# Performance work log

Hardware: AMD Instinct MI355X
Metric: run time of the kernel (lower is better)

Reference implementation:

```python
import jax, jax.numpy as jnp
import numpy as np

EPS = 1e-5

def _bn(x, gamma, beta):
    # BatchNorm with track_running_stats=False: batch stats over all dims but last
    axes = tuple(range(x.ndim - 1))
    mu = jnp.mean(x, axis=axes)
    var = jnp.var(x, axis=axes)  # biased, as torch uses for normalization
    return (x - mu) * jax.lax.rsqrt(var + EPS) * gamma + beta

def setup_inputs() -> dict:
    B, N, D = 8, 200, 128
    key = jax.random.key(0)
    ks = jax.random.split(key, 14)
    s = 1.0 / np.sqrt(D)
    def w(k):
        return jax.random.uniform(k, (D, D), jnp.float32, -s, s)
    def b(k):
        return jax.random.uniform(k, (D,), jnp.float32, -s, s)
    return {
        'h': jax.random.normal(ks[0], (B, N, D), jnp.float32),
        'e': jax.random.normal(ks[1], (B, N, N, D), jnp.float32),
        'Uw': w(ks[2]), 'Ub': b(ks[3]),
        'Vw': w(ks[4]), 'Vb': b(ks[5]),
        'Aw': w(ks[6]), 'Ab': b(ks[7]),
        'Bw': w(ks[8]), 'Bb': b(ks[9]),
        'Cw': w(ks[10]), 'Cb': b(ks[11]),
        'gamma_h': jnp.ones((D,), jnp.float32), 'beta_h': jnp.zeros((D,), jnp.float32),
        'gamma_e': jnp.ones((D,), jnp.float32), 'beta_e': jnp.zeros((D,), jnp.float32),
    }

def reference(h, e, Uw, Ub, Vw, Vb, Aw, Ab, Bw, Bb, Cw, Cb,
              gamma_h, beta_h, gamma_e, beta_e):
    h_in, e_in = h, e
    Uh = h @ Uw.T + Ub                      # [B,N,D]
    Vh = h @ Vw.T + Vb                      # [B,N,D]
    Ah = h @ Aw.T + Ab
    Bh = h @ Bw.T + Bb
    Ce = e @ Cw.T + Cb                      # [B,N,N,D]
    # e_new[b,i,j,d] = Ah[b,j,d] + Bh[b,i,d] + Ce[b,i,j,d]
    e_new = Ah[:, None, :, :] + Bh[:, :, None, :] + Ce
    gates = jax.nn.sigmoid(e_new)           # [B,N,N,D]
    # sum aggregation over source nodes j with Vh broadcast over i
    agg = jnp.sum(gates * Vh[:, None, :, :], axis=2)  # [B,N,D]
    h_new = Uh + agg
    h_out = h_in + jax.nn.relu(_bn(h_new, gamma_h, beta_h))
    e_out = e_in + jax.nn.relu(_bn(e_new, gamma_e, beta_e))
    return (h_out, e_out)
```

## Files before the change

kernel.cpp:

```cpp
#include <hip/hip_runtime.h>
#include <hip/hip_bf16.h>


#define B_ 8
#define N_ 200
#define D_ 128
#define BN_ (B_*N_)
#define HN_ (BN_*D_)

typedef __attribute__((ext_vector_type(8))) short short8v;
typedef __attribute__((ext_vector_type(4))) short short4v;
typedef __attribute__((ext_vector_type(4))) float float4v;
typedef __attribute__((ext_vector_type(4))) unsigned int uint4v;

__device__ __forceinline__ unsigned short f2b(float f) {
  unsigned u = __float_as_uint(f);
  u += 0x7FFFu + ((u >> 16) & 1u);
  return (unsigned short)(u >> 16);
}

__global__ __launch_bounds__(256) void prelin_kernel(
    const float* __restrict__ h,
    const float* __restrict__ Uw, const float* __restrict__ Ub,
    const float* __restrict__ Vw, const float* __restrict__ Vb,
    const float* __restrict__ Aw, const float* __restrict__ Ab,
    const float* __restrict__ Bw, const float* __restrict__ Bb,
    const float* __restrict__ Cw,
    float* __restrict__ Uh, float* __restrict__ Vh,
    float* __restrict__ Ah, float* __restrict__ Bh,
    unsigned short* __restrict__ Cwf) {
  const int tid = threadIdx.x;
  if (blockIdx.x >= 100) {
    const int slot = (blockIdx.x - 100) * 256 + tid;
    const int fr = slot >> 6, ln = slot & 63;
    const int t = fr >> 2, l = fr & 3, cc = ln & 15, qq = ln >> 4;
    const float* src = Cw + (t * 16 + cc) * 128 + l * 32 + qq * 8;
    float4v v0 = *(const float4v*)src;
    float4v v1 = *(const float4v*)(src + 4);
    short8v s;
    s[0] = (short)f2b(v0.x); s[1] = (short)f2b(v0.y);
    s[2] = (short)f2b(v0.z); s[3] = (short)f2b(v0.w);
    s[4] = (short)f2b(v1.x); s[5] = (short)f2b(v1.y);
    s[6] = (short)f2b(v1.z); s[7] = (short)f2b(v1.w);
    *(short8v*)(Cwf + (size_t)slot * 8) = s;
    return;
  }
  const int r0 = blockIdx.x * 16;
  __shared__ float hs[16][128];
  for (int k = 0; k < 2; k++) {
    int g = k * 256 + tid;
    int row = g >> 5, col4 = g & 31;
    *(float4v*)&hs[row][col4 * 4] =
        *(const float4v*)(h + (size_t)(r0 + row) * D_ + col4 * 4);
  }
  __syncthreads();
  const int c0 = tid, c1 = tid + 256;
  const float* w0 = (c0 < 128) ? (Uw + c0 * 128) : (Vw + (c0 - 128) * 128);
  const float  b0 = (c0 < 128) ? Ub[c0] : Vb[c0 - 128];
  const float* w1 = (c1 < 384) ? (Aw + (c1 - 256) * 128) : (Bw + (c1 - 384) * 128);
  const float  b1 = (c1 < 384) ? Ab[c1 - 256] : Bb[c1 - 384];
  float acc0[16], acc1[16];
#pragma unroll
  for (int r = 0; r < 16; r++) { acc0[r] = 0.f; acc1[r] = 0.f; }
  for (int k = 0; k < 128; k += 4) {
    float4v w0v = *(const float4v*)(w0 + k);
    float4v w1v = *(const float4v*)(w1 + k);
#pragma unroll
    for (int r = 0; r < 16; r++) {
      float4v hv = *(const float4v*)&hs[r][k];
      acc0[r] = fmaf(hv.x, w0v.x, fmaf(hv.y, w0v.y, fmaf(hv.z, w0v.z, fmaf(hv.w, w0v.w, acc0[r]))));
      acc1[r] = fmaf(hv.x, w1v.x, fmaf(hv.y, w1v.y, fmaf(hv.z, w1v.z, fmaf(hv.w, w1v.w, acc1[r]))));
    }
  }
  float* dst0 = (c0 < 128) ? Uh : Vh; const int cc0 = c0 & 127;
  float* dst1 = (c1 < 384) ? Ah : Bh; const int cc1 = (c1 - 256) & 127;
#pragma unroll
  for (int r = 0; r < 16; r++) {
    dst0[(size_t)(r0 + r) * D_ + cc0] = acc0[r] + b0;
    dst1[(size_t)(r0 + r) * D_ + cc1] = acc1[r] + b1;
  }
}

template <int MODE>
__global__ __launch_bounds__(256, 4) void gemm_pass(
    const float* __restrict__ e, const unsigned short* __restrict__ Cwf,
    const float* __restrict__ Cb, const float* __restrict__ Ah,
    const float* __restrict__ Bh, const float* __restrict__ Vh,
    float* __restrict__ agg, float* __restrict__ psum, float* __restrict__ psumsq,
    const float* __restrict__ scale_e, const float* __restrict__ shift_e,
    float* __restrict__ e_out) {
  const int tid = threadIdx.x;
  const int blk = blockIdx.x;
  const int bi = blk >> 2, jt = blk & 3;
  const int b = bi / N_;
  const int lane = tid & 63, wz = tid >> 6;
  const int c = lane & 15, q = lane >> 4;
  const int j0 = jt * 64;

  __shared__ __align__(16) unsigned short Bs[16384];
  __shared__ float base_s[128];
  __shared__ float ss_s[256];

  const int jrow = j0 + wz * 16 + c;
  const bool rok = (jrow < N_);
  const float* ep = e + ((size_t)bi * N_ + jrow) * D_ + q * 8;
  float4v ef[8];
#pragma unroll
  for (int l = 0; l < 4; l++) {
    ef[2 * l]     = rok ? *(const float4v*)(ep + l * 32)     : (float4v){0.f,0.f,0.f,0.f};
    ef[2 * l + 1] = rok ? *(const float4v*)(ep + l * 32 + 4) : (float4v){0.f,0.f,0.f,0.f};
  }

  {
    const uint4v* bsrc = (const uint4v*)Cwf;
    uint4v* bdst = (uint4v*)Bs;
#pragma unroll
    for (int k2 = 0; k2 < 8; k2++) bdst[k2 * 256 + tid] = bsrc[k2 * 256 + tid];
  }
  if (tid < 128) {
    base_s[tid] = Cb[tid] + Bh[(size_t)bi * D_ + tid];
    if (MODE == 1) { ss_s[tid] = scale_e[tid]; ss_s[128 + tid] = shift_e[tid]; }
  }

  short8v av[4];
#pragma unroll
  for (int l = 0; l < 4; l++) {
    float4v v0 = ef[2 * l], v1 = ef[2 * l + 1];
    short8v s;
    s[0] = (short)f2b(v0.x); s[1] = (short)f2b(v0.y);
    s[2] = (short)f2b(v0.z); s[3] = (short)f2b(v0.w);
    s[4] = (short)f2b(v1.x); s[5] = (short)f2b(v1.y);
    s[6] = (short)f2b(v1.z); s[7] = (short)f2b(v1.w);
    av[l] = s;
  }
  __syncthreads();

  float4v acc[8];
#pragma unroll
  for (int t = 0; t < 8; t++) acc[t] = (float4v){0.f, 0.f, 0.f, 0.f};
#pragma unroll
  for (int l = 0; l < 4; l++) {
#pragma unroll
    for (int t = 0; t < 8; t++) {
      short8v cw = *(const short8v*)&Bs[(((t * 4 + l) * 64) + lane) * 8];
      if (MODE == 0)
        acc[t] = __builtin_amdgcn_mfma_f32_16x16x32_bf16(av[l], cw, acc[t], 0, 0, 0);
      else
        acc[t] = __builtin_amdgcn_mfma_f32_16x16x32_bf16(cw, av[l], acc[t], 0, 0, 0);
    }
  }

  if (MODE == 0) {
    const float* AhB = Ah + (size_t)b * N_ * D_;
    const float* VhB = Vh + (size_t)b * N_ * D_;
#pragma unroll
    for (int t = 0; t < 8; t++) {
      const int n = t * 16 + c;
      const float bse = base_s[n];
      float at = 0.f, st = 0.f, qt = 0.f;
#pragma unroll
      for (int r = 0; r < 4; r++) {
        const int j = j0 + wz * 16 + q * 4 + r;
        if (j < N_) {
          float x = acc[t][r] + bse + AhB[(size_t)j * D_ + n];
          float g = __builtin_amdgcn_rcpf(1.0f + __expf(-x));
          at += g * VhB[(size_t)j * D_ + n];
          st += x; qt += x * x;
        }
      }
      at += __shfl_xor(at, 16); at += __shfl_xor(at, 32);
      st += __shfl_xor(st, 16); st += __shfl_xor(st, 32);
      qt += __shfl_xor(qt, 16); qt += __shfl_xor(qt, 32);
      if (lane < 16) {
        atomicAdd(&agg[(size_t)bi * D_ + n], at);
        atomicAdd(&psum[(size_t)bi * D_ + n], st);
        atomicAdd(&psumsq[(size_t)bi * D_ + n], qt);
      }
    }
  } else {
    const int j = j0 + wz * 16 + c;
    if (j < N_) {
      const float* AhB = Ah + (size_t)b * N_ * D_;
      const size_t rowoff = ((size_t)bi * N_ + j) * D_;
#pragma unroll
      for (int t = 0; t < 8; t++) {
        const int n4 = t * 16 + q * 4;
        float4v ah = *(const float4v*)(AhB + (size_t)j * D_ + n4);
        float4v bs4 = *(const float4v*)&base_s[n4];
        float4v sc4 = *(const float4v*)&ss_s[n4];
        float4v sh4 = *(const float4v*)&ss_s[128 + n4];
        float4v ein = *(const float4v*)(e + rowoff + n4);
        float4v o;
#pragma unroll
        for (int r = 0; r < 4; r++) {
          float x = acc[t][r] + bs4[r] + ah[r];
          float y = fmaxf(x * sc4[r] + sh4[r], 0.f);
          o[r] = ein[r] + y;
        }
        *(float4v*)(e_out + rowoff + n4) = o;
      }
    }
  }
}

__global__ __launch_bounds__(256) void stats_part(
    const float* __restrict__ psum, const float* __restrict__ psumsq,
    const float* __restrict__ Uh, const float* __restrict__ agg,
    float* __restrict__ partial) {
  const int t = threadIdx.x, blk = blockIdx.x;
  const int cg = t & 31, rs = t >> 5;
  float4v ps = {0,0,0,0}, pq = {0,0,0,0}, hs = {0,0,0,0}, hq = {0,0,0,0};
#pragma unroll
  for (int p = 0; p < 2; p++) {
    const int row = blk * 16 + p * 8 + rs;
    const size_t off = (size_t)row * D_ + cg * 4;
    float4v a = *(const float4v*)(psum + off);
    float4v bq = *(const float4v*)(psumsq + off);
    float4v u = *(const float4v*)(Uh + off);
    float4v g = *(const float4v*)(agg + off);
    ps += a; pq += bq;
    float4v hv = u + g;
    hs += hv; hq += hv * hv;
  }
  __shared__ float4v red[4][8][32];
  red[0][rs][cg] = ps; red[1][rs][cg] = pq; red[2][rs][cg] = hs; red[3][rs][cg] = hq;
  __syncthreads();
  if (t < 128) {
    const int s = t >> 5, g = t & 31;
    float4v acc = red[s][0][g];
#pragma unroll
    for (int r = 1; r < 8; r++) acc += red[s][r][g];
    *(float4v*)(partial + (size_t)blk * 512 + s * 128 + g * 4) = acc;
  }
}

__global__ __launch_bounds__(128) void stats_final(
    const float* __restrict__ partial,
    const float* __restrict__ gamma_h, const float* __restrict__ beta_h,
    const float* __restrict__ gamma_e, const float* __restrict__ beta_e,
    float* __restrict__ scale_e, float* __restrict__ shift_e,
    float* __restrict__ scale_h, float* __restrict__ shift_h) {
  const int n = threadIdx.x;
  float s = 0.f, sq = 0.f, hs = 0.f, hq = 0.f;
  for (int p = 0; p < 100; p++) {
    const float* base = partial + (size_t)p * 512;
    s += base[n]; sq += base[128 + n]; hs += base[256 + n]; hq += base[384 + n];
  }
  const float Me = 8.f * 200.f * 200.f;
  float mean = s / Me;
  float var = sq / Me - mean * mean;
  float sce = gamma_e[n] * rsqrtf(var + 1e-5f);
  scale_e[n] = sce; shift_e[n] = beta_e[n] - mean * sce;
  const float Mh = (float)BN_;
  float mh = hs / Mh;
  float vh = hq / Mh - mh * mh;
  float sch = gamma_h[n] * rsqrtf(vh + 1e-5f);
  scale_h[n] = sch; shift_h[n] = beta_h[n] - mh * sch;
}

__global__ __launch_bounds__(256) void hpath_kernel(
    const float* __restrict__ h, const float* __restrict__ Uh,
    const float* __restrict__ agg, const float* __restrict__ scale_h,
    const float* __restrict__ shift_h, float* __restrict__ h_out) {
  const int idx = blockIdx.x * 256 + threadIdx.x;
  float4v u = ((const float4v*)Uh)[idx];
  float4v a = ((const float4v*)agg)[idx];
  float4v hv = ((const float4v*)h)[idx];
  float4v sc = ((const float4v*)scale_h)[idx & 31];
  float4v sh = ((const float4v*)shift_h)[idx & 31];
  float4v o;
#pragma unroll
  for (int l = 0; l < 4; l++) {
    float y = fmaxf((u[l] + a[l]) * sc[l] + sh[l], 0.f);
    o[l] = hv[l] + y;
  }
  ((float4v*)h_out)[idx] = o;
}

extern "C" void kernel_launch(void* const* d_in, const int* in_sizes, int n_in,
                              void* d_out, int out_size, void* d_ws, size_t ws_size,
                              hipStream_t stream) {
  const float* h  = (const float*)d_in[0];
  const float* e  = (const float*)d_in[1];
  const float* Uw = (const float*)d_in[2];  const float* Ub = (const float*)d_in[3];
  const float* Vw = (const float*)d_in[4];  const float* Vb = (const float*)d_in[5];
  const float* Aw = (const float*)d_in[6];  const float* Ab = (const float*)d_in[7];
  const float* Bw = (const float*)d_in[8];  const float* Bb = (const float*)d_in[9];
  const float* Cw = (const float*)d_in[10]; const float* Cb = (const float*)d_in[11];
  const float* gamma_h = (const float*)d_in[12]; const float* beta_h = (const float*)d_in[13];
  const float* gamma_e = (const float*)d_in[14]; const float* beta_e = (const float*)d_in[15];

  float* ws = (float*)d_ws;
  float* Uh = ws + 0;
  float* Vh = ws + (size_t)HN_;
  float* Ah = ws + (size_t)HN_ * 2;
  float* Bh = ws + (size_t)HN_ * 3;
  float* agg = ws + (size_t)HN_ * 4;
  float* psum = ws + (size_t)HN_ * 5;
  float* psumsq = ws + (size_t)HN_ * 6;
  float* scale_e = ws + (size_t)HN_ * 7;
  float* shift_e = scale_e + 128;
  float* scale_h = scale_e + 256;
  float* shift_h = scale_e + 384;
  unsigned short* Cwf = (unsigned short*)(scale_e + 512);
  float* partial = scale_e + 512 + 8192;

  float* h_out = (float*)d_out;
  float* e_out = (float*)d_out + HN_;

  prelin_kernel<<<108, 256, 0, stream>>>(h, Uw, Ub, Vw, Vb, Aw, Ab, Bw, Bb, Cw,
                                         Uh, Vh, Ah, Bh, Cwf);
  hipMemsetAsync(agg, 0, (size_t)3 * HN_ * sizeof(float), stream);
  gemm_pass<0><<<BN_ * 4, 256, 0, stream>>>(e, Cwf, Cb, Ah, Bh, Vh,
                                            agg, psum, psumsq,
                                            nullptr, nullptr, nullptr);
  stats_part<<<100, 256, 0, stream>>>(psum, psumsq, Uh, agg, partial);
  stats_final<<<1, 128, 0, stream>>>(partial, gamma_h, beta_h, gamma_e, beta_e,
                                     scale_e, shift_e, scale_h, shift_h);
  hpath_kernel<<<200, 256, 0, stream>>>(h, Uh, agg, scale_h, shift_h, h_out);
  gemm_pass<1><<<BN_ * 4, 256, 0, stream>>>(e, Cwf, Cb, Ah, Bh, nullptr,
                                            nullptr, nullptr, nullptr,
                                            scale_e, shift_e, e_out);
}
```

Baseline: 495.1 us.

## Process a whole (b,i) row per block with register-prefetched e tiles

Each block now handles all 200 j rows of one (b,i) pair instead of a quarter of them. Each wave loops over four 16-row groups and prefetches the next group's e values into registers while the current one runs through MFMA. Per-row reductions are combined in shared memory and written directly, which removes the memset and the global atomics. The Cw tile is loaded into LDS once per row rather than four times, but the grid has four times fewer blocks and each thread holds more registers, which may reduce occupancy and latency hiding.

```diff
diff --git a/kernel.cpp b/kernel.cpp
--- a/kernel.cpp
+++ b/kernel.cpp
@@ -90,26 +90,16 @@
     const float* __restrict__ scale_e, const float* __restrict__ shift_e,
     float* __restrict__ e_out) {
   const int tid = threadIdx.x;
-  const int blk = blockIdx.x;
-  const int bi = blk >> 2, jt = blk & 3;
+  const int bi = blockIdx.x;
   const int b = bi / N_;
-  const int lane = tid & 63, wz = tid >> 6;
+  const int lane = tid & 63, wv = tid >> 6;
   const int c = lane & 15, q = lane >> 4;
-  const int j0 = jt * 64;
+  const int j0 = wv * 64;
 
   __shared__ __align__(16) unsigned short Bs[16384];
   __shared__ float base_s[128];
   __shared__ float ss_s[256];
-
-  const int jrow = j0 + wz * 16 + c;
-  const bool rok = (jrow < N_);
-  const float* ep = e + ((size_t)bi * N_ + jrow) * D_ + q * 8;
-  float4v ef[8];
-#pragma unroll
-  for (int l = 0; l < 4; l++) {
-    ef[2 * l]     = rok ? *(const float4v*)(ep + l * 32)     : (float4v){0.f,0.f,0.f,0.f};
-    ef[2 * l + 1] = rok ? *(const float4v*)(ep + l * 32 + 4) : (float4v){0.f,0.f,0.f,0.f};
-  }
+  __shared__ float red[3][4][128];
 
   {
     const uint4v* bsrc = (const uint4v*)Cwf;
@@ -122,83 +112,145 @@
     if (MODE == 1) { ss_s[tid] = scale_e[tid]; ss_s[128 + tid] = shift_e[tid]; }
   }
 
-  short8v av[4];
-#pragma unroll
-  for (int l = 0; l < 4; l++) {
-    float4v v0 = ef[2 * l], v1 = ef[2 * l + 1];
-    short8v s;
-    s[0] = (short)f2b(v0.x); s[1] = (short)f2b(v0.y);
-    s[2] = (short)f2b(v0.z); s[3] = (short)f2b(v0.w);
-    s[4] = (short)f2b(v1.x); s[5] = (short)f2b(v1.y);
-    s[6] = (short)f2b(v1.z); s[7] = (short)f2b(v1.w);
-    av[l] = s;
+  const float* eb = e + (size_t)bi * N_ * D_;
+  const float* AhB = Ah + (size_t)b * N_ * D_;
+  const float* VhB = (MODE == 0) ? (Vh + (size_t)b * N_ * D_) : nullptr;
+
+  float4v ef[8];
+  {
+    const int j = j0 + c;
+    const bool ok = (j < N_);
+    const float* p = eb + (size_t)j * D_ + q * 8;
+#pragma unroll
+    for (int l = 0; l < 4; l++) {
+      ef[2 * l]     = ok ? *(const float4v*)(p + l * 32)     : (float4v){0.f,0.f,0.f,0.f};
+      ef[2 * l + 1] = ok ? *(const float4v*)(p + l * 32 + 4) : (float4v){0.f,0.f,0.f,0.f};
+    }
   }
   __syncthreads();
 
-  float4v acc[8];
-#pragma unroll
-  for (int t = 0; t < 8; t++) acc[t] = (float4v){0.f, 0.f, 0.f, 0.f};
-#pragma unroll
-  for (int l = 0; l < 4; l++) {
+  float at[8], st[8], qt[8], bse[8];
+  if (MODE == 0) {
 #pragma unroll
     for (int t = 0; t < 8; t++) {
-      short8v cw = *(const short8v*)&Bs[(((t * 4 + l) * 64) + lane) * 8];
-      if (MODE == 0)
-        acc[t] = __builtin_amdgcn_mfma_f32_16x16x32_bf16(av[l], cw, acc[t], 0, 0, 0);
-      else
-        acc[t] = __builtin_amdgcn_mfma_f32_16x16x32_bf16(cw, av[l], acc[t], 0, 0, 0);
+      at[t] = 0.f; st[t] = 0.f; qt[t] = 0.f;
+      bse[t] = base_s[t * 16 + c];
+    }
+  }
+
+#pragma unroll
+  for (int g = 0; g < 4; g++) {
+    const int jg = j0 + g * 16;
+    if (jg < N_) {
+      short8v av[4];
+#pragma unroll
+      for (int l = 0; l < 4; l++) {
+        float4v v0 = ef[2 * l], v1 = ef[2 * l + 1];
+        short8v s;
+        s[0] = (short)f2b(v0.x); s[1] = (short)f2b(v0.y);
+        s[2] = (short)f2b(v0.z); s[3] = (short)f2b(v0.w);
+        s[4] = (short)f2b(v1.x); s[5] = (short)f2b(v1.y);
+        s[6] = (short)f2b(v1.z); s[7] = (short)f2b(v1.w);
+        av[l] = s;
+      }
+      float4v efn[8];
+      if (g < 3) {
+        const int j = jg + 16 + c;
+        const bool ok = (j < N_);
+        const float* p = eb + (size_t)j * D_ + q * 8;
+#pragma unroll
+        for (int l = 0; l < 4; l++) {
+          efn[2 * l]     = ok ? *(const float4v*)(p + l * 32)     : (float4v){0.f,0.f,0.f,0.f};
+          efn[2 * l + 1] = ok ? *(const float4v*)(p + l * 32 + 4) : (float4v){0.f,0.f,0.f,0.f};
+        }
+      }
+
+      float4v acc[8];
+#pragma unroll
+      for (int t = 0; t < 8; t++) acc[t] = (float4v){0.f, 0.f, 0.f, 0.f};
+#pragma unroll
+      for (int l = 0; l < 4; l++) {
+#pragma unroll
+        for (int t = 0; t < 8; t++) {
+          short8v cw = *(const short8v*)&Bs[(((t * 4 + l) * 64) + lane) * 8];
+          if (MODE == 0)
+            acc[t] = __builtin_amdgcn_mfma_f32_16x16x32_bf16(av[l], cw, acc[t], 0, 0, 0);
+          else
+            acc[t] = __builtin_amdgcn_mfma_f32_16x16x32_bf16(cw, av[l], acc[t], 0, 0, 0);
+        }
+      }
+
+      if (MODE == 0) {
+#pragma unroll
+        for (int t = 0; t < 8; t++) {
+          const int n = t * 16 + c;
+#pragma unroll
+          for (int r = 0; r < 4; r++) {
+            const int j = jg + q * 4 + r;
+            if (j < N_) {
+              float x = acc[t][r] + bse[t] + AhB[(size_t)j * D_ + n];
+              float gg = __builtin_amdgcn_rcpf(1.0f + __expf(-x));
+              at[t] += gg * VhB[(size_t)j * D_ + n];
+              st[t] += x; qt[t] += x * x;
+            }
+          }
+        }
+      } else {
+        const int j = jg + c;
+        if (j < N_) {
+          const size_t rowoff = ((size_t)bi * N_ + j) * D_;
+#pragma unroll
+          for (int t = 0; t < 8; t++) {
+            const int n4 = t * 16 + q * 4;
+            float4v ah = *(const float4v*)(AhB + (size_t)j * D_ + n4);
+            float4v bs4 = *(const float4v*)&base_s[n4];
+            float4v sc4 = *(const float4v*)&ss_s[n4];
+            float4v sh4 = *(const float4v*)&ss_s[128 + n4];
+            float4v ein = *(const float4v*)(e + rowoff + n4);
+            float4v o;
+#pragma unroll
+            for (int r = 0; r < 4; r++) {
+              float x = acc[t][r] + bs4[r] + ah[r];
+              float y = fmaxf(x * sc4[r] + sh4[r], 0.f);
+              o[r] = ein[r] + y;
+            }
+            *(float4v*)(e_out + rowoff + n4) = o;
+          }
+        }
+      }
+
+      if (g < 3) {
+#pragma unroll
+        for (int i = 0; i < 8; i++) ef[i] = efn[i];
+      }
     }
   }
 
   if (MODE == 0) {
-    const float* AhB = Ah + (size_t)b * N_ * D_;
-    const float* VhB = Vh + (size_t)b * N_ * D_;
 #pragma unroll
     for (int t = 0; t < 8; t++) {
-      const int n = t * 16 + c;
-      const float bse = base_s[n];
-      float at = 0.f, st = 0.f, qt = 0.f;
-#pragma unroll
-      for (int r = 0; r < 4; r++) {
-        const int j = j0 + wz * 16 + q * 4 + r;
-        if (j < N_) {
-          float x = acc[t][r] + bse + AhB[(size_t)j * D_ + n];
-          float g = __builtin_amdgcn_rcpf(1.0f + __expf(-x));
-          at += g * VhB[(size_t)j * D_ + n];
-          st += x; qt += x * x;
-        }
-      }
-      at += __shfl_xor(at, 16); at += __shfl_xor(at, 32);
-      st += __shfl_xor(st, 16); st += __shfl_xor(st, 32);
-      qt += __shfl_xor(qt, 16); qt += __shfl_xor(qt, 32);
-      if (lane < 16) {
-        atomicAdd(&agg[(size_t)bi * D_ + n], at);
-        atomicAdd(&psum[(size_t)bi * D_ + n], st);
-        atomicAdd(&psumsq[(size_t)bi * D_ + n], qt);
-      }
-    }
-  } else {
-    const int j = j0 + wz * 16 + c;
-    if (j < N_) {
-      const float* AhB = Ah + (size_t)b * N_ * D_;
-      const size_t rowoff = ((size_t)bi * N_ + j) * D_;
-#pragma unroll
-      for (int t = 0; t < 8; t++) {
-        const int n4 = t * 16 + q * 4;
-        float4v ah = *(const float4v*)(AhB + (size_t)j * D_ + n4);
-        float4v bs4 = *(const float4v*)&base_s[n4];
-        float4v sc4 = *(const float4v*)&ss_s[n4];
-        float4v sh4 = *(const float4v*)&ss_s[128 + n4];
-        float4v ein = *(const float4v*)(e + rowoff + n4);
-        float4v o;
-#pragma unroll
-        for (int r = 0; r < 4; r++) {
-          float x = acc[t][r] + bs4[r] + ah[r];
-          float y = fmaxf(x * sc4[r] + sh4[r], 0.f);
-          o[r] = ein[r] + y;
-        }
-        *(float4v*)(e_out + rowoff + n4) = o;
-      }
+      float a = at[t], s = st[t], sq = qt[t];
+      a += __shfl_xor(a, 16); a += __shfl_xor(a, 32);
+      s += __shfl_xor(s, 16); s += __shfl_xor(s, 32);
+      sq += __shfl_xor(sq, 16); sq += __shfl_xor(sq, 32);
+      if (q == 0) {
+        red[0][wv][t * 16 + c] = a;
+        red[1][wv][t * 16 + c] = s;
+        red[2][wv][t * 16 + c] = sq;
+      }
+    }
+    __syncthreads();
+    if (tid < 128) {
+      float a = 0.f, s = 0.f, sq = 0.f;
+#pragma unroll
+      for (int w = 0; w < 4; w++) {
+        a += red[0][w][tid];
+        s += red[1][w][tid];
+        sq += red[2][w][tid];
+      }
+      agg[(size_t)bi * D_ + tid] = a;
+      psum[(size_t)bi * D_ + tid] = s;
+      psumsq[(size_t)bi * D_ + tid] = sq;
     }
   }
 }
@@ -310,15 +362,14 @@
 
   prelin_kernel<<<108, 256, 0, stream>>>(h, Uw, Ub, Vw, Vb, Aw, Ab, Bw, Bb, Cw,
                                          Uh, Vh, Ah, Bh, Cwf);
-  hipMemsetAsync(agg, 0, (size_t)3 * HN_ * sizeof(float), stream);
-  gemm_pass<0><<<BN_ * 4, 256, 0, stream>>>(e, Cwf, Cb, Ah, Bh, Vh,
-                                            agg, psum, psumsq,
-                                            nullptr, nullptr, nullptr);
+  gemm_pass<0><<<BN_, 256, 0, stream>>>(e, Cwf, Cb, Ah, Bh, Vh,
+                                        agg, psum, psumsq,
+                                        nullptr, nullptr, nullptr);
   stats_part<<<100, 256, 0, stream>>>(psum, psumsq, Uh, agg, partial);
   stats_final<<<1, 128, 0, stream>>>(partial, gamma_h, beta_h, gamma_e, beta_e,
                                      scale_e, shift_e, scale_h, shift_h);
   hpath_kernel<<<200, 256, 0, stream>>>(h, Uh, agg, scale_h, shift_h, h_out);
-  gemm_pass<1><<<BN_ * 4, 256, 0, stream>>>(e, Cwf, Cb, Ah, Bh, nullptr,
-                                            nullptr, nullptr, nullptr,
-                                            scale_e, shift_e, e_out);
-}
+  gemm_pass<1><<<BN_, 256, 0, stream>>>(e, Cwf, Cb, Ah, Bh, nullptr,
+                                        nullptr, nullptr, nullptr,
+                                        scale_e, shift_e, e_out);
+}
```

Measured after the change: 515.9 us. +4.2%, slower.
